# Kernel optimization log

Measured on AMD Instinct MI355X. Metric: run time of the kernel, lower is better.

The kernel has to match this reference:

```python
import jax, jax.numpy as jnp
import numpy as np

N, DIM, R, C = 1024, 201, 72, 4


def setup_inputs() -> dict:
    key = jax.random.key(0)
    k1, k2 = jax.random.split(key)
    x = jax.random.normal(k1, (N, DIM, R, C), dtype=jnp.float32)
    labels = jax.random.randint(k2, (N, R, C), 0, 201, dtype=jnp.int64)
    return {"x": x, "labels": labels}


def _parse_top_down(labels, G):
    # Faithful vectorization of the triple python loop:
    #   top  = first row index with a valid label (label < G); empty if none
    #   down = 0 if rows 0->1 is a valid->invalid transition,
    #          else R-1 if last row valid,
    #          else first valid->invalid transition index; empty if no valid row.
    # (top empty <=> down empty <=> no valid row; then both forced to 0)
    R = labels.shape[1]
    valid = labels < G                              # [n, R, C]
    any_valid = valid.any(axis=1)                   # [n, C]
    first_valid = jnp.argmax(valid, axis=1)         # [n, C]
    trans = valid[:, :-1] & ~valid[:, 1:]           # [n, R-1, C] valid->invalid
    any_trans = trans.any(axis=1)
    first_trans = jnp.argmax(trans, axis=1)
    down = jnp.where(trans[:, 0], 0,
                     jnp.where(valid[:, -1], R - 1,
                               jnp.where(any_trans, first_trans, 0)))
    top = jnp.where(any_valid, first_valid, 0)
    down = jnp.where(any_valid, down, 0)
    return top, down                                # [n, C] each


def _lane_loss(x, labels):
    n, dim, R, C = x.shape
    G = dim - 1
    # softmax-weighted expected grid position per (image, row, lane)
    p = jax.nn.softmax(x[:, :G], axis=1)
    emb = jnp.arange(G, dtype=x.dtype).reshape(1, G, 1, 1)
    pos = jnp.sum(p * emb, axis=1)                  # [n, R, C]

    top, down = _parse_top_down(labels, G)

    # second difference across lanes: d_i - d_{i+1} = pos_i - 2 pos_{i+1} + pos_{i+2}
    dd = jnp.abs(pos[:, :, :-2] - 2.0 * pos[:, :, 1:-1] + pos[:, :, 2:])  # [n, R, C-2]
    rows = jnp.arange(R)

    def side(lane_lo, lane_hi, col_lo, col_hi):
        t = jnp.max(top[:, lane_lo:lane_hi], axis=1)   # [n]
        d = jnp.min(down[:, lane_lo:lane_hi], axis=1)  # [n]
        active = t < d
        W = (d - t + 1).astype(x.dtype)                # segment length
        mask = ((rows[None, :] >= t[:, None]) & (rows[None, :] <= d[:, None])).astype(x.dtype)
        s = jnp.einsum('nr,nrc->n', mask, dd[:, :, col_lo:col_hi])
        Wsafe = jnp.where(active, W, 1.0)
        npairs = float(col_hi - col_lo)                # == C-3 pairs of diffs
        # L1 mean over W rows, then /W again, then / (num pairs)
        loss = jnp.where(active, s / (Wsafe * Wsafe) / npairs, 0.0)
        w = jnp.where(active, W, 0.0)
        return loss, w, active

    loss_l, w_l, left = side(0, 3, 0, C - 3)
    loss_r, w_r, right = side(1, 4, 1, C - 2)
    denom = jnp.where(left & right, 2.0 * R, float(R))
    loss_k = (loss_l * w_l + loss_r * w_r) / denom     # [n]
    flag = jnp.sum((loss_k != 0).astype(jnp.int32))
    total = jnp.sum(loss_k)
    return jnp.where(flag > 0, total / flag.astype(x.dtype), jnp.asarray(0.0, x.dtype))


def reference(x, labels):
    return _lane_loss(x, labels)
```

## Files before the change

kernel.cpp:

```cpp
#include <hip/hip_runtime.h>

#define NIMG  1024
#define DIMX  201
#define GVAL  200
#define RROW  72
#define CLN   4
#define COLS  (RROW * CLN)

__global__ __launch_bounds__(320) void lane_loss_main(
    const float* __restrict__ x, const int* __restrict__ labels,
    float* __restrict__ total, int* __restrict__ flag)
{
    __shared__ float         pos_s[COLS];
    __shared__ unsigned char valid_s[COLS];
    __shared__ int           td_s[8];

    const int n   = blockIdx.x;
    const int tid = threadIdx.x;

    if (tid < COLS) {
        int lab = labels[n * COLS + tid];
        valid_s[tid] = (lab < GVAL) ? 1 : 0;

        const float* xp = x + (size_t)n * (DIMX * COLS) + tid;
        float s = 0.f, ws = 0.f, df = 0.f;
        #pragma unroll 4
        for (int d = 0; d < GVAL; ++d) {
            float v = xp[d * COLS];
            float e = __expf(v);
            s += e;
            ws = fmaf(df, e, ws);
            df += 1.f;
        }
        pos_s[tid] = ws / s;
    }
    __syncthreads();

    if (tid < CLN) {
        const int c = tid;
        bool any_valid = false; int first_valid = 0;
        bool any_trans = false; int first_trans = 0;
        bool trans0 = false;
        bool v_prev = (valid_s[c] != 0);
        if (v_prev) { any_valid = true; first_valid = 0; }
        for (int r = 1; r < RROW; ++r) {
            bool v = (valid_s[r * CLN + c] != 0);
            if (v && !any_valid) { any_valid = true; first_valid = r; }
            bool tr = v_prev && !v;
            if (tr && !any_trans) { any_trans = true; first_trans = r - 1; }
            if (r == 1) trans0 = tr;
            v_prev = v;
        }
        bool valid_last = v_prev;
        int down;
        if (trans0)          down = 0;
        else if (valid_last) down = RROW - 1;
        else if (any_trans)  down = first_trans;
        else                 down = 0;
        int top = any_valid ? first_valid : 0;
        if (!any_valid) down = 0;
        td_s[c]     = top;
        td_s[4 + c] = down;
    }
    __syncthreads();

    if (tid < 64) {
        const int t_l = max(td_s[0], max(td_s[1], td_s[2]));
        const int d_l = min(td_s[4], min(td_s[5], td_s[6]));
        const int t_r = max(td_s[1], max(td_s[2], td_s[3]));
        const int d_r = min(td_s[5], min(td_s[6], td_s[7]));

        float sl = 0.f, sr = 0.f;
        for (int r = tid; r < RROW; r += 64) {
            float p0 = pos_s[r * 4 + 0];
            float p1 = pos_s[r * 4 + 1];
            float p2 = pos_s[r * 4 + 2];
            float p3 = pos_s[r * 4 + 3];
            float ddl = fabsf(p0 - 2.f * p1 + p2);
            float ddr = fabsf(p1 - 2.f * p2 + p3);
            if (r >= t_l && r <= d_l) sl += ddl;
            if (r >= t_r && r <= d_r) sr += ddr;
        }
        #pragma unroll
        for (int off = 32; off > 0; off >>= 1) {
            sl += __shfl_down(sl, off, 64);
            sr += __shfl_down(sr, off, 64);
        }
        if (tid == 0) {
            bool aL = (t_l < d_l), aR = (t_r < d_r);
            float WL = (float)(d_l - t_l + 1);
            float WR = (float)(d_r - t_r + 1);
            float ll = aL ? (sl / WL) : 0.f;
            float lr = aR ? (sr / WR) : 0.f;
            float denom = (aL && aR) ? (2.f * (float)RROW) : (float)RROW;
            float lk = (ll + lr) / denom;
            if (lk != 0.f) {
                atomicAdd(total, lk);
                atomicAdd(flag, 1);
            }
        }
    }
}

__global__ void lane_loss_finalize(const float* __restrict__ total,
                                   const int* __restrict__ flag,
                                   float* __restrict__ out)
{
    if (blockIdx.x == 0 && threadIdx.x == 0) {
        int f = *flag;
        out[0] = (f > 0) ? (*total / (float)f) : 0.f;
    }
}

extern "C" void kernel_launch(void* const* d_in, const int* in_sizes, int n_in,
                              void* d_out, int out_size, void* d_ws, size_t ws_size,
                              hipStream_t stream)
{
    const float* x      = (const float*)d_in[0];
    const int*   labels = (const int*)d_in[1];
    float*       out    = (float*)d_out;

    float* total = (float*)d_ws;
    int*   flag  = (int*)((char*)d_ws + sizeof(float));

    hipMemsetAsync(d_ws, 0, 2 * sizeof(float), stream);

    lane_loss_main<<<NIMG, 320, 0, stream>>>(x, labels, total, flag);
    lane_loss_finalize<<<1, 64, 0, stream>>>(total, flag, out);
}
```

Baseline: 343.2 us.

## Split softmax reduction over class slices with float4 loads and LDS combine

Each thread now handles four adjacent columns with float4 loads over one quarter of the class dimension, and the four slice partials are combined through shared memory. The block size drops from 320 to 288 threads so every thread does work. This shortens the serial dependency chain per thread and widens the memory transactions on the bandwidth-bound read of x. The cost is extra shared memory and one more barrier.

```diff
diff --git a/kernel.cpp b/kernel.cpp
--- a/kernel.cpp
+++ b/kernel.cpp
@@ -6,33 +6,53 @@
 #define RROW  72
 #define CLN   4
 #define COLS  (RROW * CLN)
+#define NSL   4
+#define NGRP  (COLS / 4)
 
-__global__ __launch_bounds__(320) void lane_loss_main(
+__global__ __launch_bounds__(COLS) void lane_loss_main(
     const float* __restrict__ x, const int* __restrict__ labels,
     float* __restrict__ total, int* __restrict__ flag)
 {
-    __shared__ float         pos_s[COLS];
+    __shared__ float s_lds[NSL][COLS];
+    __shared__ float w_lds[NSL][COLS];
+    __shared__ float pos_s[COLS];
     __shared__ unsigned char valid_s[COLS];
-    __shared__ int           td_s[8];
+    __shared__ int td_s[8];
 
     const int n   = blockIdx.x;
     const int tid = threadIdx.x;
 
-    if (tid < COLS) {
+    {
         int lab = labels[n * COLS + tid];
         valid_s[tid] = (lab < GVAL) ? 1 : 0;
+    }
 
-        const float* xp = x + (size_t)n * (DIMX * COLS) + tid;
-        float s = 0.f, ws = 0.f, df = 0.f;
-        #pragma unroll 4
-        for (int d = 0; d < GVAL; ++d) {
-            float v = xp[d * COLS];
-            float e = __expf(v);
-            s += e;
-            ws = fmaf(df, e, ws);
-            df += 1.f;
-        }
-        pos_s[tid] = ws / s;
+    const int slice = tid / NGRP;
+    const int g     = tid - slice * NGRP;
+
+    const float* xp = x + (size_t)n * (DIMX * COLS) + g * 4;
+    float4 sa = make_float4(0.f, 0.f, 0.f, 0.f);
+    float4 wa = make_float4(0.f, 0.f, 0.f, 0.f);
+    float df = (float)slice;
+    #pragma unroll 5
+    for (int d = slice; d < GVAL; d += NSL) {
+        float4 v = *(const float4*)(xp + (size_t)d * COLS);
+        float ex = __expf(v.x), ey = __expf(v.y),
+              ez = __expf(v.z), ew = __expf(v.w);
+        sa.x += ex;              sa.y += ey;
+        sa.z += ez;              sa.w += ew;
+        wa.x = fmaf(df, ex, wa.x); wa.y = fmaf(df, ey, wa.y);
+        wa.z = fmaf(df, ez, wa.z); wa.w = fmaf(df, ew, wa.w);
+        df += (float)NSL;
+    }
+    ((float4*)s_lds[slice])[g] = sa;
+    ((float4*)w_lds[slice])[g] = wa;
+    __syncthreads();
+
+    {
+        float st = s_lds[0][tid] + s_lds[1][tid] + s_lds[2][tid] + s_lds[3][tid];
+        float wt = w_lds[0][tid] + w_lds[1][tid] + w_lds[2][tid] + w_lds[3][tid];
+        pos_s[tid] = wt / st;
     }
     __syncthreads();
 
@@ -125,6 +145,6 @@
 
     hipMemsetAsync(d_ws, 0, 2 * sizeof(float), stream);
 
-    lane_loss_main<<<NIMG, 320, 0, stream>>>(x, labels, total, flag);
+    lane_loss_main<<<NIMG, COLS, 0, stream>>>(x, labels, total, flag);
     lane_loss_finalize<<<1, 64, 0, stream>>>(total, flag, out);
 }
```

New measurement: 328.2 us. 1.05x faster.
